# Kernel optimization log

Measured on AMD Instinct MI355X. Metric: run time of the kernel, lower is better.

## Reference

```python
import jax, jax.numpy as jnp
import numpy as np

N_RAYS = 65536
M_SAMPLES = 16777216  # avg ~256 samples per ray, irregular segment lengths


def setup_inputs() -> dict:
    key = jax.random.key(0)
    k1, k2, k3 = jax.random.split(key, 3)
    density = jax.random.normal(k1, (M_SAMPLES,), dtype=jnp.float32)
    rgb = jax.random.uniform(k2, (M_SAMPLES, 3), dtype=jnp.float32)
    bg = jnp.ones((3,), dtype=jnp.float32)
    # use_mipnerf_density=True -> act_shift = -1; interval = voxel_size_ratio * stepsize
    shift = jnp.float32(-1.0)
    interval = jnp.float32(0.5)
    ray_id = jnp.sort(jax.random.randint(k3, (M_SAMPLES,), 0, N_RAYS, dtype=jnp.int32))
    return {"density": density, "rgb": rgb, "bg": bg, "shift": shift,
            "interval": interval, "ray_id": ray_id, "n_rays": N_RAYS}


def _segmented_exclusive_cumsum(x, flags):
    """Exclusive cumsum of x restarting wherever flags is True (segment starts)."""
    def combine(a, b):
        xa, fa = a
        xb, fb = b
        return (jnp.where(fb, xb, xa + xb), fa | fb)
    inc, _ = jax.lax.associative_scan(combine, (x, flags))
    return inc - x


def reference(density, rgb, bg, shift, interval, ray_id, n_rays):
    # Raw2Alpha: alpha = 1 - (1 + exp(density + shift)) ** (-interval)
    #   => log(1 - alpha) = -interval * softplus(density + shift)  (exact)
    log_trans = -jax.nn.softplus(density + shift) * interval      # [M] log(1-alpha)
    alpha = -jnp.expm1(log_trans)                                  # [M]

    # Alphas2Weights: per-ray exclusive cumprod of (1 - alpha)
    flags = jnp.concatenate([jnp.ones((1,), bool), ray_id[1:] != ray_id[:-1]])
    logT = _segmented_exclusive_cumsum(log_trans, flags)           # [M] log T_i
    weights = alpha * jnp.exp(logT)                                # [M]
    seg_tot = jax.ops.segment_sum(log_trans, ray_id, num_segments=n_rays)
    alphainv_last = jnp.exp(seg_tot)                               # [N] final transmittance

    # Alpha compositing with background
    rgb_marched = jax.ops.segment_sum(weights[:, None] * rgb, ray_id,
                                      num_segments=n_rays)
    rgb_marched = rgb_marched + alphainv_last[:, None] * bg[None, :]  # [N,3]
    return rgb_marched
```

## Files before the change

kernel.cpp:

```cpp
#include <hip/hip_runtime.h>
#include <math.h>

__global__ void seg_starts_kernel(const int* __restrict__ ray_id, int M, int N,
                                  int* __restrict__ seg_start) {
    int r = blockIdx.x * blockDim.x + threadIdx.x;
    if (r > N) return;
    int lo = 0, hi = M;
    while (lo < hi) {
        int mid = (lo + hi) >> 1;
        if (ray_id[mid] < r) lo = mid + 1;
        else hi = mid;
    }
    seg_start[r] = lo;
}

__launch_bounds__(256, 4)
__global__ void composite_kernel(const float* __restrict__ density,
                                 const float* __restrict__ rgb,
                                 const float* __restrict__ bg,
                                 const float* __restrict__ shift_p,
                                 const float* __restrict__ interval_p,
                                 const int* __restrict__ seg_start,
                                 float* __restrict__ out, int N) {
    const int wave = threadIdx.x >> 6;
    const int lane = threadIdx.x & 63;
    const int r = blockIdx.x * (blockDim.x >> 6) + wave;
    if (r >= N) return;

    const float shift = *shift_p;
    const float interval = *interval_p;
    const int s = seg_start[r];
    const int e = seg_start[r + 1];

    float T = 1.0f;
    float ar = 0.f, ag = 0.f, ab = 0.f;

    for (int base = s; base < e; base += 64) {
        int i = base + lane;
        float t1 = 1.0f;
        float cr = 0.f, cg = 0.f, cb = 0.f;
        if (i < e) {
            float x = density[i] + shift;
            float sp = (x > 20.0f) ? x : log1pf(__expf(x));
            t1 = __expf(-interval * sp);
            cr = rgb[3 * i + 0];
            cg = rgb[3 * i + 1];
            cb = rgb[3 * i + 2];
        }
        float p = t1;
        #pragma unroll
        for (int off = 1; off < 64; off <<= 1) {
            float o = __shfl_up(p, off);
            if (lane >= off) p *= o;
        }
        float excl = __shfl_up(p, 1);
        if (lane == 0) excl = 1.0f;
        float w = T * (excl - p);
        ar += w * cr;
        ag += w * cg;
        ab += w * cb;
        T *= __shfl(p, 63);
    }

    #pragma unroll
    for (int off = 32; off > 0; off >>= 1) {
        ar += __shfl_xor(ar, off);
        ag += __shfl_xor(ag, off);
        ab += __shfl_xor(ab, off);
    }

    if (lane == 0) {
        out[3 * r + 0] = ar + T * bg[0];
        out[3 * r + 1] = ag + T * bg[1];
        out[3 * r + 2] = ab + T * bg[2];
    }
}

extern "C" void kernel_launch(void* const* d_in, const int* in_sizes, int n_in,
                              void* d_out, int out_size, void* d_ws, size_t ws_size,
                              hipStream_t stream) {
    const float* density  = (const float*)d_in[0];
    const float* rgb      = (const float*)d_in[1];
    const float* bg       = (const float*)d_in[2];
    const float* shift    = (const float*)d_in[3];
    const float* interval = (const float*)d_in[4];
    const int*   ray_id   = (const int*)d_in[5];

    const int M = in_sizes[0];
    const int N = out_size / 3;

    int* seg_start = (int*)d_ws;

    {
        int threads = 256;
        int blocks = (N + 1 + threads - 1) / threads;
        seg_starts_kernel<<<blocks, threads, 0, stream>>>(ray_id, M, N, seg_start);
    }
    {
        const int wavesPerBlock = 4;
        int blocks = (N + wavesPerBlock - 1) / wavesPerBlock;
        composite_kernel<<<blocks, 256, 0, stream>>>(density, rgb, bg, shift,
                                                     interval, seg_start,
                                                     (float*)d_out, N);
    }
}
```

Measured before the change: 375.3 us.

## Process two samples per lane with vectorized loads and early ray termination

Each lane now handles two consecutive samples, so each wave scan covers 128 samples. Loads use float2 for density and rgb from an even-aligned base, and the compositing weights are rewritten algebraically per pair. This halves the number of shuffle-scan passes and widens the loads. The loop also exits once transmittance drops below 1e-9, skipping the remaining samples of a ray, which slightly approximates the reference.

```diff
diff --git a/kernel.cpp b/kernel.cpp
--- a/kernel.cpp
+++ b/kernel.cpp
@@ -12,6 +12,12 @@
         else hi = mid;
     }
     seg_start[r] = lo;
+}
+
+__device__ __forceinline__ float transmit(float d, float shift, float interval) {
+    float x = d + shift;
+    float sp = (x > 20.0f) ? x : log1pf(__expf(x));
+    return __expf(-interval * sp);
 }
 
 __launch_bounds__(256, 4)
@@ -35,19 +41,33 @@
     float T = 1.0f;
     float ar = 0.f, ag = 0.f, ab = 0.f;
 
-    for (int base = s; base < e; base += 64) {
-        int i = base + lane;
-        float t1 = 1.0f;
-        float cr = 0.f, cg = 0.f, cb = 0.f;
-        if (i < e) {
-            float x = density[i] + shift;
-            float sp = (x > 20.0f) ? x : log1pf(__expf(x));
-            t1 = __expf(-interval * sp);
-            cr = rgb[3 * i + 0];
-            cg = rgb[3 * i + 1];
-            cb = rgb[3 * i + 2];
+    for (int base = (s & ~1); base < e; base += 128) {
+        int j0 = base + 2 * lane;
+        float t0 = 1.f, t1 = 1.f;
+        float r0 = 0.f, g0 = 0.f, b0 = 0.f, r1 = 0.f, g1 = 0.f, b1 = 0.f;
+
+        if (j0 >= s && j0 + 1 < e) {
+            float2 d2 = *(const float2*)(density + j0);
+            t0 = transmit(d2.x, shift, interval);
+            t1 = transmit(d2.y, shift, interval);
+            const float2* rg = (const float2*)(rgb + 3 * j0);
+            float2 p0 = rg[0], p1 = rg[1], p2 = rg[2];
+            r0 = p0.x; g0 = p0.y; b0 = p1.x;
+            r1 = p1.y; g1 = p2.x; b1 = p2.y;
+        } else {
+            if (j0 >= s && j0 < e) {
+                t0 = transmit(density[j0], shift, interval);
+                r0 = rgb[3 * j0 + 0]; g0 = rgb[3 * j0 + 1]; b0 = rgb[3 * j0 + 2];
+            }
+            int j1 = j0 + 1;
+            if (j1 >= s && j1 < e) {
+                t1 = transmit(density[j1], shift, interval);
+                r1 = rgb[3 * j1 + 0]; g1 = rgb[3 * j1 + 1]; b1 = rgb[3 * j1 + 2];
+            }
         }
-        float p = t1;
+
+        float q = t0 * t1;
+        float p = q;
         #pragma unroll
         for (int off = 1; off < 64; off <<= 1) {
             float o = __shfl_up(p, off);
@@ -55,11 +75,13 @@
         }
         float excl = __shfl_up(p, 1);
         if (lane == 0) excl = 1.0f;
-        float w = T * (excl - p);
-        ar += w * cr;
-        ag += w * cg;
-        ab += w * cb;
+        float Tl = T * excl;
+        ar += Tl * ((1.f - t0) * r0 + (t0 - q) * r1);
+        ag += Tl * ((1.f - t0) * g0 + (t0 - q) * g1);
+        ab += Tl * ((1.f - t0) * b0 + (t0 - q) * b1);
+
         T *= __shfl(p, 63);
+        if (T < 1e-9f) break;
     }
 
     #pragma unroll
```

Result: faster. 341.0 us (-9.1%).
